# Kernel optimization log

Hardware: AMD Instinct MI355X
Metric: run time of the kernel (lower is better)

Reference implementation:

```python
import jax, jax.numpy as jnp
import numpy as np

N_HEADS = 16

def setup_inputs() -> dict:
    key = jax.random.key(0)
    qkv = jax.random.normal(key, (4, 3072, 2048), dtype=jnp.float32)
    return {"qkv": qkv}

def reference(qkv) -> jnp.ndarray:
    bs, width, length = qkv.shape
    ch = width // (3 * N_HEADS)
    # [bs*H, 3*ch, T] -> split into q, k, v each [bs*H, ch, T]
    qkv_r = qkv.reshape(bs * N_HEADS, 3 * ch, length)
    q, k, v = qkv_r[:, :ch], qkv_r[:, ch:2 * ch], qkv_r[:, 2 * ch:]
    scale = 1.0 / jnp.sqrt(jnp.sqrt(jnp.float32(ch)))
    # scores: [bs*H, T, T]
    weight = jnp.einsum('bct,bcs->bts', q * scale, k * scale)
    weight = jax.nn.softmax(weight.astype(jnp.float32), axis=-1).astype(weight.dtype)
    a = jnp.einsum('bts,bcs->bct', weight, v)  # [bs*H, ch, T]
    return a.reshape(bs, N_HEADS * ch, length)
```

## Files before the change

kernel.cpp:

```cpp
#include <hip/hip_runtime.h>

namespace {

constexpr int D  = 64;
constexpr int T  = 2048;
constexpr int TQ = 64;
constexpr int NT = T / 64;
constexpr float SCL = 0.125f * 1.44269504088896340736f;

constexpr size_t QP_OFF  = (size_t)64 * 32 * 8192;
constexpr size_t WS_NEED = ((size_t)64 * 32 * 8192 + (size_t)64 * 32 * 4096) * 2;

typedef __bf16 bf16x8 __attribute__((ext_vector_type(8)));
typedef float  f32x4  __attribute__((ext_vector_type(4)));
typedef unsigned short u16x4 __attribute__((ext_vector_type(4)));
typedef unsigned short u16x8 __attribute__((ext_vector_type(8)));
typedef unsigned int   u32x2 __attribute__((ext_vector_type(2)));
typedef short          s16x4 __attribute__((ext_vector_type(4)));

__device__ inline unsigned short f2bf(float f) {
    unsigned int u = __builtin_bit_cast(unsigned int, f);
    u += 0x7FFFu + ((u >> 16) & 1u);
    return (unsigned short)(u >> 16);
}

__device__ inline unsigned int pkbf(float a, float b) {
#if __has_builtin(__builtin_amdgcn_cvt_pk_bf16_f32)
    auto r = __builtin_amdgcn_cvt_pk_bf16_f32(a, b);
    static_assert(sizeof(r) == 4, "cvt_pk_bf16 size");
    return __builtin_bit_cast(unsigned int, r);
#else
    return (unsigned int)f2bf(a) | ((unsigned int)f2bf(b) << 16);
#endif
}

__device__ inline int frag_off(int row, int c0) {
    int g = (c0 >> 3) ^ ((row >> 1) & 7);
    return row * 64 + g * 8;
}

__device__ inline void async_cp16(const void* g, void* l) {
    __builtin_amdgcn_global_load_lds(
        (const __attribute__((address_space(1))) unsigned int*)g,
        (__attribute__((address_space(3))) unsigned int*)l, 16, 0, 0);
}

__global__ __launch_bounds__(256)
void prepass(const float* __restrict__ qkv, unsigned short* __restrict__ ws) {
    const int tile = blockIdx.x, h = blockIdx.y, z = blockIdx.z;
    const int tid = threadIdx.x;
    const float* src = qkv + (size_t)h * 3 * D * T + (size_t)z * D * T + tile * 64;
    __shared__ unsigned short L[4096];

    if (z == 2) {
        unsigned short* dst = ws + (size_t)(h * 32 + tile) * 8192 + 4096;
        const int c = tid >> 2, g = tid & 3;
        const int sg = g ^ ((c >> 2) & 3);
        #pragma unroll
        for (int wq = 0; wq < 4; wq++) {
            f32x4 a = *(const f32x4*)(src + (size_t)c * T + wq * 16 + sg * 4);
            u16x4 wv = { f2bf(a[0]), f2bf(a[1]), f2bf(a[2]), f2bf(a[3]) };
            *(u16x4*)(dst + wq * 1024 + tid * 4) = wv;
        }
    } else {
        const float m = (z == 0) ? SCL : 1.0f;
        const int c0 = (tid >> 4) * 4, s4 = tid & 15;
        float fr[4][4];
        #pragma unroll
        for (int r = 0; r < 4; r++)
            *(f32x4*)fr[r] = *(const f32x4*)(src + (size_t)(c0 + r) * T + s4 * 4);
        #pragma unroll
        for (int j = 0; j < 4; j++) {
            int trow = s4 * 4 + j;
            u16x4 wv = { f2bf(fr[0][j] * m), f2bf(fr[1][j] * m),
                         f2bf(fr[2][j] * m), f2bf(fr[3][j] * m) };
            *(u16x4*)(L + frag_off(trow, c0) + (c0 & 7)) = wv;
        }
        __syncthreads();
        unsigned short* dst = (z == 0)
            ? ws + QP_OFF + (size_t)(h * 32 + tile) * 4096
            : ws + (size_t)(h * 32 + tile) * 8192;
        #pragma unroll
        for (int i = 0; i < 2; i++)
            *(u16x8*)(dst + tid * 16 + i * 8) = *(const u16x8*)(L + tid * 16 + i * 8);
    }
}


#define STAGE(J, B)                                                          \
  { const char* g = kvb + (size_t)(J) * 16384;                               \
    char* lk = lbase + (B) * 16384;                                          \
    async_cp16(g,         lk);                                               \
    async_cp16(g + 4096,  lk + 4096);                                        \
    async_cp16(g + 8192,  lk + 8192);                                        \
    async_cp16(g + 12288, lk + 12288); }

#define BODY(KT, B, DO_STAGE, WAITIMM)                                       \
  {                                                                          \
    __builtin_amdgcn_s_waitcnt(WAITIMM);         \
    __builtin_amdgcn_s_barrier();             \
    __builtin_amdgcn_sched_barrier(0);          \
    _Pragma("unroll")                                                        \
    for (int q = 0; q < 4; q++) {                                            \
      const char* kb = sbuf + (B) * 16384 + q * 2048;                        \
      const char* vb = sbuf + (B) * 16384 + 8192 + q * 2048;                 \
      bf16x8 aK0 = *(const bf16x8*)(kb + aK0o);                              \
      bf16x8 aK1 = *(const bf16x8*)(kb + aK1o);                              \
      s16x4 aV0 = *(const s16x4*)(vb + aVo);                                 \
      s16x4 aV1 = *(const s16x4*)(vb + aVo + 512);                           \
      s16x4 aV2 = *(const s16x4*)(vb + aVo + 1024);                          \
      s16x4 aV3 = *(const s16x4*)(vb + aVo + 1536);                          \
      f32x4 s = __builtin_amdgcn_mfma_f32_16x16x32_bf16(aK0, bQ0, ZF, 0,0,0);\
      s = __builtin_amdgcn_mfma_f32_16x16x32_bf16(aK1, bQ1, s, 0, 0, 0);     \
      float p0 = __builtin_amdgcn_exp2f(s[0]);                               \
      float p1 = __builtin_amdgcn_exp2f(s[1]);                               \
      float p2 = __builtin_amdgcn_exp2f(s[2]);                               \
      float p3 = __builtin_amdgcn_exp2f(s[3]);                               \
      l_acc += (p0 + p1) + (p2 + p3);                                        \
      u32x2 pk = { pkbf(p0, p1), pkbf(p2, p3) };                             \
      s16x4 bP = __builtin_bit_cast(s16x4, pk);                              \
      acc_o[0] = __builtin_amdgcn_mfma_f32_16x16x16bf16_1k(                  \
          aV0, bP, acc_o[0], 0, 0, 0);                                       \
      acc_o[1] = __builtin_amdgcn_mfma_f32_16x16x16bf16_1k(                  \
          aV1, bP, acc_o[1], 0, 0, 0);                                       \
      acc_o[2] = __builtin_amdgcn_mfma_f32_16x16x16bf16_1k(                  \
          aV2, bP, acc_o[2], 0, 0, 0);                                       \
      acc_o[3] = __builtin_amdgcn_mfma_f32_16x16x16bf16_1k(                  \
          aV3, bP, acc_o[3], 0, 0, 0);                                       \
    }                                                                        \
    if (DO_STAGE) {                                                          \
      __builtin_amdgcn_s_waitcnt(0xC07F);        \
      __builtin_amdgcn_s_barrier();           \
      STAGE((KT) + 2, B)                                                     \
    }                                                                        \
  }

__global__ __launch_bounds__(256, 4)
void attn_main(const unsigned short* __restrict__ ws, float* __restrict__ out) {
    const int h  = blockIdx.x;
    const int qt = blockIdx.y;
    const int t0 = qt * TQ;
    const int tid  = threadIdx.x;
    const int lane = tid & 63;
    const int w    = tid >> 6;
    const int ln   = lane & 15, q4 = lane >> 4;

    __shared__ char sbuf[32768];
    char* lbase = sbuf + w * 1024;

    const int aK0o = 2 * frag_off(ln, q4 * 8);
    const int aK1o = 2 * frag_off(ln, 32 + q4 * 8);
    const int aVo  = 32 * ln + 2 * ((q4 ^ ((ln >> 2) & 3)) * 4);

    const unsigned short* qtile = ws + QP_OFF + (size_t)(h * 32 + qt) * 4096;
    bf16x8 bQ0 = *(const bf16x8*)(qtile + frag_off(16 * w + ln, q4 * 8));
    bf16x8 bQ1 = *(const bf16x8*)(qtile + frag_off(16 * w + ln, 32 + q4 * 8));

    const char* kvb = (const char*)ws + (size_t)(h * 32) * 16384
                      + w * 1024 + lane * 16;
    STAGE(0, 0)
    STAGE(1, 1)

    const f32x4 ZF = {0.f, 0.f, 0.f, 0.f};
    f32x4 acc_o[4] = {ZF, ZF, ZF, ZF};
    float l_acc = 0.f;

    #pragma unroll 1
    for (int m = 0; m < 15; m++) {
        BODY(2 * m,     0, 1, 0x0F74)
        BODY(2 * m + 1, 1, 1, 0x0F74)
    }
    BODY(30, 0, 0, 0x0F74)
    BODY(31, 1, 0, 0x0F70)

    float sl = l_acc;
    sl += __shfl_xor(sl, 16, 64);
    sl += __shfl_xor(sl, 32, 64);
    const float linv = 1.0f / sl;
    float* ob = out + (size_t)h * D * T + t0 + 16 * w + ln;
    #pragma unroll
    for (int ci = 0; ci < 4; ci++)
        #pragma unroll
        for (int rr = 0; rr < 4; rr++)
            ob[(size_t)(16 * ci + q4 * 4 + rr) * T] = acc_o[ci][rr] * linv;
}

__device__ inline bf16x8 frag8(const unsigned short* p, int row, int c0) {
    return *(const bf16x8*)(p + frag_off(row, c0));
}

__global__ __launch_bounds__(256)
void attn_fallback(const float* __restrict__ qkv, float* __restrict__ out) {
    const int h     = blockIdx.y;
    const int t0    = blockIdx.x * TQ;
    const int tid   = threadIdx.x;
    const int lane  = tid & 63;
    const int strip = tid >> 6;
    const int ln    = lane & 15;
    const int q4    = lane >> 4;

    __shared__ unsigned short Qs[TQ * D];
    __shared__ unsigned short Ks[64 * D];
    __shared__ unsigned short Vs[D * 64];
    __shared__ unsigned short Pss[TQ * 64];
    __shared__ float l_lds[TQ];

    const float* qb = qkv + (size_t)h * 3 * D * T;
    const float* kb = qb + (size_t)D * T;
    const float* vb = qb + (size_t)(2 * D) * T;
    const int s4 = tid & 15;
    const int c0 = (tid >> 4) * 4;
    {
        float fr[4][4];
        #pragma unroll
        for (int r = 0; r < 4; r++)
            *(f32x4*)fr[r] = *(const f32x4*)(qb + (size_t)(c0 + r) * T + t0 + s4 * 4);
        #pragma unroll
        for (int j = 0; j < 4; j++) {
            int trow = s4 * 4 + j;
            u16x4 wv = { f2bf(fr[0][j]), f2bf(fr[1][j]), f2bf(fr[2][j]), f2bf(fr[3][j]) };
            *(u16x4*)(Qs + frag_off(trow, c0) + (c0 & 7)) = wv;
        }
    }
    __syncthreads();
    const int arow = strip * 16 + ln;
    const int kg   = q4 * 8;
    const bf16x8 aq0 = frag8(Qs, arow, kg);
    const bf16x8 aq1 = frag8(Qs, arow, 32 + kg);
    f32x4 acc_o[4];
    #pragma unroll
    for (int m = 0; m < 4; m++) acc_o[m] = (f32x4){0.f, 0.f, 0.f, 0.f};
    float l_acc[4] = {0.f, 0.f, 0.f, 0.f};
    constexpr float S2 = 0.125f * 1.44269504088896340736f;
    for (int kt = 0; kt < NT; kt++) {
        const int s0 = kt * 64;
        float kr[4][4], vr[4][4];
        #pragma unroll
        for (int r = 0; r < 4; r++)
            *(f32x4*)kr[r] = *(const f32x4*)(kb + (size_t)(c0 + r) * T + s0 + s4 * 4);
        #pragma unroll
        for (int r = 0; r < 4; r++)
            *(f32x4*)vr[r] = *(const f32x4*)(vb + (size_t)(c0 + r) * T + s0 + s4 * 4);
        __syncthreads();
        #pragma unroll
        for (int j = 0; j < 4; j++) {
            int srow = s4 * 4 + j;
            u16x4 wk = { f2bf(kr[0][j]), f2bf(kr[1][j]), f2bf(kr[2][j]), f2bf(kr[3][j]) };
            *(u16x4*)(Ks + frag_off(srow, c0) + (c0 & 7)) = wk;
        }
        #pragma unroll
        for (int r = 0; r < 4; r++) {
            int row = c0 + r, cc = s4 * 4;
            u16x4 wv = { f2bf(vr[r][0]), f2bf(vr[r][1]), f2bf(vr[r][2]), f2bf(vr[r][3]) };
            *(u16x4*)(Vs + frag_off(row, cc) + (cc & 7)) = wv;
        }
        __syncthreads();
        f32x4 accs[4];
        #pragma unroll
        for (int ns = 0; ns < 4; ns++) {
            bf16x8 b0 = frag8(Ks, ns * 16 + ln, kg);
            bf16x8 b1 = frag8(Ks, ns * 16 + ln, 32 + kg);
            f32x4 z = {0.f, 0.f, 0.f, 0.f};
            z = __builtin_amdgcn_mfma_f32_16x16x32_bf16(aq0, b0, z, 0, 0, 0);
            z = __builtin_amdgcn_mfma_f32_16x16x32_bf16(aq1, b1, z, 0, 0, 0);
            accs[ns] = z;
        }
        #pragma unroll
        for (int ns = 0; ns < 4; ns++) {
            int scol = ns * 16 + ln;
            #pragma unroll
            for (int r = 0; r < 4; r++) {
                float p = __builtin_amdgcn_exp2f(accs[ns][r] * S2);
                l_acc[r] += p;
                int trow = strip * 16 + q4 * 4 + r;
                int g = ((scol >> 3) ^ ((trow >> 1) & 7));
                Pss[trow * 64 + g * 8 + (scol & 7)] = f2bf(p);
            }
        }
        bf16x8 bp0 = frag8(Pss, arow, kg);
        bf16x8 bp1 = frag8(Pss, arow, 32 + kg);
        #pragma unroll
        for (int ms = 0; ms < 4; ms++) {
            bf16x8 av0 = frag8(Vs, ms * 16 + ln, kg);
            bf16x8 av1 = frag8(Vs, ms * 16 + ln, 32 + kg);
            acc_o[ms] = __builtin_amdgcn_mfma_f32_16x16x32_bf16(av0, bp0, acc_o[ms], 0, 0, 0);
            acc_o[ms] = __builtin_amdgcn_mfma_f32_16x16x32_bf16(av1, bp1, acc_o[ms], 0, 0, 0);
        }
    }
    #pragma unroll
    for (int r = 0; r < 4; r++) {
        float s = l_acc[r];
        s += __shfl_xor(s, 1, 64);
        s += __shfl_xor(s, 2, 64);
        s += __shfl_xor(s, 4, 64);
        s += __shfl_xor(s, 8, 64);
        if (ln == 0) l_lds[strip * 16 + q4 * 4 + r] = s;
    }
    const float linv = 1.0f / l_lds[strip * 16 + ln];
    const int tg = t0 + strip * 16 + ln;
    float* ob = out + (size_t)h * D * T;
    #pragma unroll
    for (int ms = 0; ms < 4; ms++)
        #pragma unroll
        for (int r = 0; r < 4; r++) {
            int c = ms * 16 + q4 * 4 + r;
            ob[(size_t)c * T + tg] = acc_o[ms][r] * linv;
        }
}

}

extern "C" void kernel_launch(void* const* d_in, const int* in_sizes, int n_in,
                              void* d_out, int out_size, void* d_ws, size_t ws_size,
                              hipStream_t stream) {
    const float* qkv = (const float*)d_in[0];
    float* out = (float*)d_out;
    if (ws_size >= WS_NEED) {
        prepass<<<dim3(32, 64, 3), 256, 0, stream>>>(qkv, (unsigned short*)d_ws);
        attn_main<<<dim3(64, 32), 256, 0, stream>>>((const unsigned short*)d_ws, out);
    } else {
        attn_fallback<<<dim3(32, 64), 256, 0, stream>>>(qkv, out);
    }
}
```

Before: 254.1 us.

## Process two query tiles per block to reuse staged K/V fragments

Each attn_main block now handles 128 queries (two 64-query sub-tiles) instead of 64, so every K/V tile staged into LDS and every K/V fragment loaded into registers feeds two sets of score and PV MFMAs. The grid is halved to 64x16 blocks. This cuts LDS staging traffic and K/V fragment loads per unit of work. In exchange it doubles accumulator and Q-fragment register use, which may hurt occupancy under the launch bounds of 4, and halves the block count to 1024.

```diff
diff --git a/kernel.cpp b/kernel.cpp
--- a/kernel.cpp
+++ b/kernel.cpp
@@ -4,7 +4,6 @@
 
 constexpr int D  = 64;
 constexpr int T  = 2048;
-constexpr int TQ = 64;
 constexpr int NT = T / 64;
 constexpr float SCL = 0.125f * 1.44269504088896340736f;
 
@@ -110,23 +109,27 @@
       s16x4 aV1 = *(const s16x4*)(vb + aVo + 512);                           \
       s16x4 aV2 = *(const s16x4*)(vb + aVo + 1024);                          \
       s16x4 aV3 = *(const s16x4*)(vb + aVo + 1536);                          \
-      f32x4 s = __builtin_amdgcn_mfma_f32_16x16x32_bf16(aK0, bQ0, ZF, 0,0,0);\
-      s = __builtin_amdgcn_mfma_f32_16x16x32_bf16(aK1, bQ1, s, 0, 0, 0);     \
-      float p0 = __builtin_amdgcn_exp2f(s[0]);                               \
-      float p1 = __builtin_amdgcn_exp2f(s[1]);                               \
-      float p2 = __builtin_amdgcn_exp2f(s[2]);                               \
-      float p3 = __builtin_amdgcn_exp2f(s[3]);                               \
-      l_acc += (p0 + p1) + (p2 + p3);                                        \
-      u32x2 pk = { pkbf(p0, p1), pkbf(p2, p3) };                             \
-      s16x4 bP = __builtin_bit_cast(s16x4, pk);                              \
-      acc_o[0] = __builtin_amdgcn_mfma_f32_16x16x16bf16_1k(                  \
-          aV0, bP, acc_o[0], 0, 0, 0);                                       \
-      acc_o[1] = __builtin_amdgcn_mfma_f32_16x16x16bf16_1k(                  \
-          aV1, bP, acc_o[1], 0, 0, 0);                                       \
-      acc_o[2] = __builtin_amdgcn_mfma_f32_16x16x16bf16_1k(                  \
-          aV2, bP, acc_o[2], 0, 0, 0);                                       \
-      acc_o[3] = __builtin_amdgcn_mfma_f32_16x16x16bf16_1k(                  \
-          aV3, bP, acc_o[3], 0, 0, 0);                                       \
+      _Pragma("unroll")                                                      \
+      for (int st = 0; st < 2; st++) {                                       \
+        f32x4 s = __builtin_amdgcn_mfma_f32_16x16x32_bf16(                   \
+            aK0, bQ[st][0], ZF, 0, 0, 0);                                    \
+        s = __builtin_amdgcn_mfma_f32_16x16x32_bf16(aK1, bQ[st][1], s, 0,0,0);\
+        float p0 = __builtin_amdgcn_exp2f(s[0]);                             \
+        float p1 = __builtin_amdgcn_exp2f(s[1]);                             \
+        float p2 = __builtin_amdgcn_exp2f(s[2]);                             \
+        float p3 = __builtin_amdgcn_exp2f(s[3]);                             \
+        l_acc[st] += (p0 + p1) + (p2 + p3);                                  \
+        u32x2 pk = { pkbf(p0, p1), pkbf(p2, p3) };                           \
+        s16x4 bP = __builtin_bit_cast(s16x4, pk);                            \
+        acc_o[st][0] = __builtin_amdgcn_mfma_f32_16x16x16bf16_1k(            \
+            aV0, bP, acc_o[st][0], 0, 0, 0);                                 \
+        acc_o[st][1] = __builtin_amdgcn_mfma_f32_16x16x16bf16_1k(            \
+            aV1, bP, acc_o[st][1], 0, 0, 0);                                 \
+        acc_o[st][2] = __builtin_amdgcn_mfma_f32_16x16x16bf16_1k(            \
+            aV2, bP, acc_o[st][2], 0, 0, 0);                                 \
+        acc_o[st][3] = __builtin_amdgcn_mfma_f32_16x16x16bf16_1k(            \
+            aV3, bP, acc_o[st][3], 0, 0, 0);                                 \
+      }                                                                      \
     }                                                                        \
     if (DO_STAGE) {                                                          \
       __builtin_amdgcn_s_waitcnt(0xC07F);        \
@@ -139,7 +142,7 @@
 void attn_main(const unsigned short* __restrict__ ws, float* __restrict__ out) {
     const int h  = blockIdx.x;
     const int qt = blockIdx.y;
-    const int t0 = qt * TQ;
+    const int t0 = qt * 128;
     const int tid  = threadIdx.x;
     const int lane = tid & 63;
     const int w    = tid >> 6;
@@ -152,9 +155,13 @@
     const int aK1o = 2 * frag_off(ln, 32 + q4 * 8);
     const int aVo  = 32 * ln + 2 * ((q4 ^ ((ln >> 2) & 3)) * 4);
 
-    const unsigned short* qtile = ws + QP_OFF + (size_t)(h * 32 + qt) * 4096;
-    bf16x8 bQ0 = *(const bf16x8*)(qtile + frag_off(16 * w + ln, q4 * 8));
-    bf16x8 bQ1 = *(const bf16x8*)(qtile + frag_off(16 * w + ln, 32 + q4 * 8));
+    const unsigned short* qtile = ws + QP_OFF + (size_t)(h * 32 + qt * 2) * 4096;
+    bf16x8 bQ[2][2];
+    #pragma unroll
+    for (int st = 0; st < 2; st++) {
+        bQ[st][0] = *(const bf16x8*)(qtile + st * 4096 + frag_off(16 * w + ln, q4 * 8));
+        bQ[st][1] = *(const bf16x8*)(qtile + st * 4096 + frag_off(16 * w + ln, 32 + q4 * 8));
+    }
 
     const char* kvb = (const char*)ws + (size_t)(h * 32) * 16384
                       + w * 1024 + lane * 16;
@@ -162,8 +169,12 @@
     STAGE(1, 1)
 
     const f32x4 ZF = {0.f, 0.f, 0.f, 0.f};
-    f32x4 acc_o[4] = {ZF, ZF, ZF, ZF};
-    float l_acc = 0.f;
+    f32x4 acc_o[2][4];
+    #pragma unroll
+    for (int st = 0; st < 2; st++)
+        #pragma unroll
+        for (int ci = 0; ci < 4; ci++) acc_o[st][ci] = ZF;
+    float l_acc[2] = {0.f, 0.f};
 
     #pragma unroll 1
     for (int m = 0; m < 15; m++) {
@@ -173,16 +184,19 @@
     BODY(30, 0, 0, 0x0F74)
     BODY(31, 1, 0, 0x0F70)
 
-    float sl = l_acc;
-    sl += __shfl_xor(sl, 16, 64);
-    sl += __shfl_xor(sl, 32, 64);
-    const float linv = 1.0f / sl;
-    float* ob = out + (size_t)h * D * T + t0 + 16 * w + ln;
-    #pragma unroll
-    for (int ci = 0; ci < 4; ci++)
-        #pragma unroll
-        for (int rr = 0; rr < 4; rr++)
-            ob[(size_t)(16 * ci + q4 * 4 + rr) * T] = acc_o[ci][rr] * linv;
+    #pragma unroll
+    for (int st = 0; st < 2; st++) {
+        float sl = l_acc[st];
+        sl += __shfl_xor(sl, 16, 64);
+        sl += __shfl_xor(sl, 32, 64);
+        const float linv = 1.0f / sl;
+        float* ob = out + (size_t)h * D * T + t0 + st * 64 + 16 * w + ln;
+        #pragma unroll
+        for (int ci = 0; ci < 4; ci++)
+            #pragma unroll
+            for (int rr = 0; rr < 4; rr++)
+                ob[(size_t)(16 * ci + q4 * 4 + rr) * T] = acc_o[st][ci][rr] * linv;
+    }
 }
 
 __device__ inline bf16x8 frag8(const unsigned short* p, int row, int c0) {
@@ -192,18 +206,18 @@
 __global__ __launch_bounds__(256)
 void attn_fallback(const float* __restrict__ qkv, float* __restrict__ out) {
     const int h     = blockIdx.y;
-    const int t0    = blockIdx.x * TQ;
+    const int t0    = blockIdx.x * 64;
     const int tid   = threadIdx.x;
     const int lane  = tid & 63;
     const int strip = tid >> 6;
     const int ln    = lane & 15;
     const int q4    = lane >> 4;
 
-    __shared__ unsigned short Qs[TQ * D];
+    __shared__ unsigned short Qs[64 * D];
     __shared__ unsigned short Ks[64 * D];
     __shared__ unsigned short Vs[D * 64];
-    __shared__ unsigned short Pss[TQ * 64];
-    __shared__ float l_lds[TQ];
+    __shared__ unsigned short Pss[64 * 64];
+    __shared__ float l_lds[64];
 
     const float* qb = qkv + (size_t)h * 3 * D * T;
     const float* kb = qb + (size_t)D * T;
@@ -317,7 +331,7 @@
     float* out = (float*)d_out;
     if (ws_size >= WS_NEED) {
         prepass<<<dim3(32, 64, 3), 256, 0, stream>>>(qkv, (unsigned short*)d_ws);
-        attn_main<<<dim3(64, 32), 256, 0, stream>>>((const unsigned short*)d_ws, out);
+        attn_main<<<dim3(64, 16), 256, 0, stream>>>((const unsigned short*)d_ws, out);
     } else {
         attn_fallback<<<dim3(32, 64), 256, 0, stream>>>(qkv, out);
     }
```

Measured after the change: 247.2 us. 1.03x faster.
